# Performance work log

Measured on AMD Instinct MI355X. Metric: run time of the kernel, lower is better.

## Reference

```python
import jax, jax.numpy as jnp
import numpy as np

# Grid / problem constants
D = H = W_SP = 128      # spatial_shape of the sparse tensor (single batch)
N = 200_000             # number of active voxels
C = 64                  # nchan
K = 5                   # SubMConv3d kernel_size
PAD = 2                 # padding (stride=1 submanifold => output sites == input sites)
EPS = 1e-5              # BatchNorm eps (torch default)


def setup_inputs() -> dict:
    key = jax.random.key(0)
    k1, k2, k3 = jax.random.split(key, 3)
    # unique active voxel coordinates: permute linear grid indices, take first N
    lin = jax.random.permutation(k1, D * H * W_SP)[:N]
    z = lin // (H * W_SP)
    y = (lin // W_SP) % H
    x = lin % W_SP
    coords = jnp.stack([z, y, x], axis=1).astype(jnp.int32)   # [N,3]
    feats = jax.random.normal(k2, (N, C), jnp.float32)        # [N,C]
    std = (2.0 / (K ** 3 * C)) ** 0.5
    Wt = jax.random.normal(k3, (K ** 3, C, C), jnp.float32) * std  # [125,Cin,Cout]
    bias = jnp.full((C,), -0.01, jnp.float32)
    gamma = jnp.ones((C,), jnp.float32)   # bn weight (init 1)
    beta = jnp.zeros((C,), jnp.float32)   # bn bias (init 0)
    return {"feats": feats, "coords": coords, "Wt": Wt, "bias": bias,
            "gamma": gamma, "beta": beta}


def _subm_conv(feats, coords, Wt, bias):
    """Submanifold sparse 3D conv: out[p] = sum_k W_k @ feat[p + off_k], active only."""
    lin = (coords[:, 0] * H + coords[:, 1]) * W_SP + coords[:, 2]
    # dense hash: grid position -> active-voxel row index (or -1)
    idx_map = jnp.full((D * H * W_SP,), -1, jnp.int32).at[lin].set(
        jnp.arange(N, dtype=jnp.int32))
    r = jnp.arange(-PAD, PAD + 1)
    offs = jnp.stack(jnp.meshgrid(r, r, r, indexing="ij"), axis=-1)
    offs = offs.reshape(-1, 3).astype(jnp.int32)              # [125,3]
    bounds = jnp.array([D, H, W_SP], jnp.int32)

    def step(acc, kw):
        Wk, off = kw                                          # [C,C], [3]
        nb = coords + off                                     # [N,3]
        valid = jnp.all((nb >= 0) & (nb < bounds), axis=1)    # [N]
        nlin = (nb[:, 0] * H + nb[:, 1]) * W_SP + nb[:, 2]
        j = idx_map[jnp.where(valid, nlin, 0)]                # [N]
        ok = valid & (j >= 0)
        f = jnp.where(ok[:, None], feats[jnp.maximum(j, 0)], 0.0)  # gather [N,C]
        return acc + f @ Wk, None

    acc0 = jnp.zeros((N, C), feats.dtype)
    out, _ = jax.lax.scan(step, acc0, (Wt, offs))
    return out + bias


def reference(feats, coords, Wt, bias, gamma, beta):
    h = _subm_conv(feats, coords, Wt, bias)
    # BatchNorm1d over active voxels (training-mode batch statistics)
    mean = h.mean(axis=0)
    var = ((h - mean) ** 2).mean(axis=0)
    h = (h - mean) * jax.lax.rsqrt(var + EPS) * gamma + beta
    return jax.nn.elu(h)
```

## Files before the change

### kernel.cpp

```cpp
#include <hip/hip_runtime.h>
#include <hip/hip_bf16.h>

#define NVOX 200000
#define NK   125
#define KG   5
#define GRID_LIN (128 * 128 * 128)

#define WT_OFF    0u
#define STATS_OFF 1024000u
#define PFX_OFF   1024512u
#define OLD_OFF   1032704u
#define FB_OFF    1832704u
#define IDX_OFF   27432832u

#define F16N   (NVOX * 16)
#define WCONV_N (NK * 4096)
#define PREP_N (F16N + 16 + WCONV_N)

typedef short bf16x8 __attribute__((ext_vector_type(8)));
typedef float f32x4  __attribute__((ext_vector_type(4)));
typedef unsigned short u16x4 __attribute__((ext_vector_type(4)));
typedef unsigned int uint_as1 __attribute__((address_space(1)));
typedef unsigned int uint_as3 __attribute__((address_space(3)));

static __device__ __forceinline__ unsigned short f2bf(float f) {
    union { float f; unsigned int u; } v; v.f = f;
    unsigned int u = v.u;
    return (unsigned short)((u + 0x7FFFu + ((u >> 16) & 1u)) >> 16);
}

__global__ __launch_bounds__(256) void scatter_kernel(const int* __restrict__ coords,
                                                      int* __restrict__ idx_map) {
    int p = blockIdx.x * 256 + threadIdx.x;
    if (p < NVOX) {
        int z = coords[p * 3 + 0], y = coords[p * 3 + 1], x = coords[p * 3 + 2];
        idx_map[(z << 14) | (y << 7) | x] = p;
    }
}

__global__ __launch_bounds__(1024) void count_kernel(const int* __restrict__ idx_map,
                                                     int* __restrict__ pfx) {
    __shared__ int wsum[16];
    int i = blockIdx.x * 1024 + threadIdx.x;
    int bit = idx_map[i] >= 0 ? 1 : 0;
    unsigned long long m = __ballot(bit);
    int lane = threadIdx.x & 63, wave = threadIdx.x >> 6;
    if (lane == 0) wsum[wave] = __popcll(m);
    __syncthreads();
    if (threadIdx.x == 0) {
        int s = 0;
#pragma unroll
        for (int w = 0; w < 16; ++w) s += wsum[w];
        pfx[blockIdx.x] = s;
    }
}

__global__ __launch_bounds__(1024) void scan_kernel(int* __restrict__ pfx) {
    __shared__ int A[2048], B[2048];
    int t = threadIdx.x;
    A[t] = pfx[t]; A[t + 1024] = pfx[t + 1024];
    __syncthreads();
    int* src = A; int* dst = B;
    for (int off = 1; off < 2048; off <<= 1) {
        dst[t]        = src[t]        + (t >= off ? src[t - off] : 0);
        dst[t + 1024] = src[t + 1024] + src[t + 1024 - off];
        __syncthreads();
        int* tmp = src; src = dst; dst = tmp;
    }
    pfx[t]        = t ? src[t - 1] : 0;
    pfx[t + 1024] = src[t + 1023];
}

__global__ __launch_bounds__(1024) void relabel_kernel(const int* __restrict__ pfx,
                                                       int* __restrict__ idx_map,
                                                       int* __restrict__ oldof) {
    __shared__ int wsum[16];
    int i = blockIdx.x * 1024 + threadIdx.x;
    int old = idx_map[i];
    int bit = old >= 0 ? 1 : 0;
    unsigned long long m = __ballot(bit);
    int lane = threadIdx.x & 63, wave = threadIdx.x >> 6;
    int intra = __popcll(m & ((1ull << lane) - 1ull));
    if (lane == 0) wsum[wave] = __popcll(m);
    __syncthreads();
    int woff = 0;
    for (int w = 0; w < wave; ++w) woff += wsum[w];
    if (bit) {
        int nid = pfx[blockIdx.x] + woff + intra;
        idx_map[i] = nid;
        oldof[nid] = old;
    }
}

__global__ __launch_bounds__(256) void prep_kernel(const float* __restrict__ Wt,
                                                   const float* __restrict__ feats,
                                                   const int* __restrict__ oldof,
                                                   unsigned short* __restrict__ wt,
                                                   unsigned short* __restrict__ fb) {
    int i = blockIdx.x * 256 + threadIdx.x;
    if (i < F16N) {
        int p = i >> 4, c = i & 15;
        int old = oldof[p];
        f32x4 f = *(const f32x4*)(feats + (size_t)old * 64 + c * 4);
        u16x4 u;
        u[0] = f2bf(f[0]); u[1] = f2bf(f[1]); u[2] = f2bf(f[2]); u[3] = f2bf(f[3]);
        *(u16x4*)(fb + (size_t)i * 4) = u;
    } else if (i < F16N + 16) {
        *(u16x4*)(fb + (size_t)i * 4) = (u16x4)0;
    } else if (i < PREP_N) {
        int j = i - (F16N + 16);
        int k = j >> 12, r = j & 4095;
        int co = r >> 6, ci = r & 63;
        int dst = (co << 6) | ((((ci >> 3) ^ (co & 7)) << 3) | (ci & 7));
        wt[(k << 12) + dst] = f2bf(Wt[(k << 12) + (ci << 6) + co]);
    }
}

static __device__ __forceinline__ void stage_w(const unsigned short* wt, int k,
                                               unsigned short* dst, int tid) {
    const unsigned short* src = wt + ((size_t)k << 12) + tid * 8;
    __builtin_amdgcn_global_load_lds((const uint_as1*)(const void*)src,
                                     (uint_as3*)(void*)(dst + tid * 8), 16, 0, 0);
    __builtin_amdgcn_global_load_lds((const uint_as1*)(const void*)(src + 2048),
                                     (uint_as3*)(void*)(dst + tid * 8 + 2048), 16, 0, 0);
}

__global__ __launch_bounds__(256, 3) void conv_kernel(
    const int* __restrict__ coords, const unsigned short* __restrict__ fb,
    const unsigned short* __restrict__ wt, const int* __restrict__ idx_map,
    const int* __restrict__ oldof,
    float* __restrict__ out, float* __restrict__ stats) {
    __shared__ unsigned short lds_w[KG * 4096];
    __shared__ int lds_nbr[KG * 256];

    const int vblk = (blockIdx.x & 7) * 98 + (blockIdx.x >> 3);
    const int vbase = vblk * 256;
    if (vbase >= NVOX) return;

    const int tid  = threadIdx.x;
    const int wave = tid >> 6;
    const int lane = tid & 63;
    const int g    = lane >> 4;
    const int l15  = lane & 15;
    const int vox  = vbase + tid;
    const bool live = vox < NVOX;

    int z = 0, y = 0, x = 0;
    if (live) {
        int old = oldof[vox];
        z = coords[old * 3 + 0]; y = coords[old * 3 + 1]; x = coords[old * 3 + 2];
    }
    const int slot = (tid & ~63) | ((tid & 15) << 2) | ((tid >> 4) & 3);
    const int sw0 = ((g    ) ^ (l15 & 7)) << 4;
    const int sw1 = ((g + 4) ^ (l15 & 7)) << 4;

    f32x4 acc[4][4];
#pragma unroll
    for (int a = 0; a < 4; ++a)
#pragma unroll
        for (int b = 0; b < 4; ++b) acc[a][b] = (f32x4)0.0f;

    const char* fbp = (const char*)fb;

    for (int grp = 0; grp < NK / KG; ++grp) {
        __syncthreads();
#pragma unroll
        for (int kk = 0; kk < KG; ++kk)
            stage_w(wt, grp * KG + kk, &lds_w[kk * 4096], tid);
        const int dz = grp / 5 - 2, dy = grp % 5 - 2;
        const int nz = z + dz, ny = y + dy;
        const bool rowok = live && ((unsigned)nz < 128u) && ((unsigned)ny < 128u);
        const int base = (nz << 14) | (ny << 7);
#pragma unroll
        for (int kk = 0; kk < KG; ++kk) {
            int nx = x + kk - 2;
            int j = NVOX;
            if (rowok && ((unsigned)nx < 128u)) {
                int t = idx_map[base | nx];
                if (t >= 0) j = t;
            }
            lds_nbr[kk * 256 + slot] = j;
        }
        __syncthreads();

        int4 jt4 = *(const int4*)&lds_nbr[wave * 64 + l15 * 4];
#pragma unroll
        for (int kk = 0; kk < KG; ++kk) {
            const int jt[4] = {jt4.x, jt4.y, jt4.z, jt4.w};

            bf16x8 b0f[4], b1f[4];
#pragma unroll
            for (int t = 0; t < 4; ++t) {
                const char* rp = fbp + ((size_t)(unsigned)jt[t] << 7) + (g << 4);
                b0f[t] = *(const bf16x8*)(rp);
                b1f[t] = *(const bf16x8*)(rp + 64);
            }
            if (kk + 1 < KG)
                jt4 = *(const int4*)&lds_nbr[(kk + 1) * 256 + wave * 64 + l15 * 4];

            const char* wb = (const char*)&lds_w[kk * 4096];
            bf16x8 af0[4], af1[4];
#pragma unroll
            for (int a = 0; a < 4; ++a) {
                af0[a] = *(const bf16x8*)(wb + (((a * 16 + l15) << 7) | sw0));
                af1[a] = *(const bf16x8*)(wb + (((a * 16 + l15) << 7) | sw1));
            }

            __builtin_amdgcn_sched_barrier(0);

#pragma unroll
            for (int t = 0; t < 4; ++t) {
                if (__any(jt[t] != NVOX)) {
#pragma unroll
                    for (int a = 0; a < 4; ++a) {
                        acc[a][t] = __builtin_amdgcn_mfma_f32_16x16x32_bf16(af0[a], b0f[t], acc[a][t], 0, 0, 0);
                        acc[a][t] = __builtin_amdgcn_mfma_f32_16x16x32_bf16(af1[a], b1f[t], acc[a][t], 0, 0, 0);
                    }
                }
            }
        }
    }

#pragma unroll
    for (int b = 0; b < 4; ++b) {
        int v = vbase + wave * 64 + b * 16 + l15;
        if (v < NVOX) {
            int o = oldof[v];
#pragma unroll
            for (int a = 0; a < 4; ++a)
                *(f32x4*)(out + (size_t)o * 64 + a * 16 + g * 4) = acc[a][b];
        }
    }

    float s1[16], s2[16];
#pragma unroll
    for (int a = 0; a < 4; ++a)
#pragma unroll
        for (int r = 0; r < 4; ++r) {
            float s = 0.f, q = 0.f;
#pragma unroll
            for (int b = 0; b < 4; ++b) { float xv = acc[a][b][r]; s += xv; q += xv * xv; }
            s1[a * 4 + r] = s; s2[a * 4 + r] = q;
        }
#pragma unroll
    for (int m = 1; m < 16; m <<= 1) {
#pragma unroll
        for (int i = 0; i < 16; ++i) {
            s1[i] += __shfl_xor(s1[i], m, 64);
            s2[i] += __shfl_xor(s2[i], m, 64);
        }
    }
    if (l15 == 0) {
#pragma unroll
        for (int a = 0; a < 4; ++a)
#pragma unroll
            for (int r = 0; r < 4; ++r) {
                int co = a * 16 + g * 4 + r;
                atomicAdd(&stats[co],      s1[a * 4 + r]);
                atomicAdd(&stats[64 + co], s2[a * 4 + r]);
            }
    }
}

__global__ __launch_bounds__(256) void finalize_kernel(float* __restrict__ out,
                                                       const float* __restrict__ stats,
                                                       const float* __restrict__ gamma,
                                                       const float* __restrict__ beta) {
    int i = blockIdx.x * 256 + threadIdx.x;
    if (i >= NVOX * 16) return;
    int cg = (i & 15) * 4;
    f32x4 v = *(f32x4*)(out + (size_t)i * 4);
    f32x4 r;
#pragma unroll
    for (int c = 0; c < 4; ++c) {
        int co = cg + c;
        float mean = stats[co] * (1.0f / NVOX);
        float var  = stats[64 + co] * (1.0f / NVOX) - mean * mean;
        float sc   = rsqrtf(var + 1e-5f) * gamma[co];
        float sh   = beta[co] - mean * sc;
        float yv   = v[c] * sc + sh;
        r[c] = yv > 0.f ? yv : expm1f(yv);
    }
    *(f32x4*)(out + (size_t)i * 4) = r;
}

extern "C" void kernel_launch(void* const* d_in, const int* in_sizes, int n_in,
                              void* d_out, int out_size, void* d_ws, size_t ws_size,
                              hipStream_t stream) {
    const float* feats  = (const float*)d_in[0];
    const int*   coords = (const int*)d_in[1];
    const float* Wt     = (const float*)d_in[2];
    const float* gamma  = (const float*)d_in[4];
    const float* beta   = (const float*)d_in[5];
    float* out = (float*)d_out;
    char*  ws  = (char*)d_ws;

    unsigned short* wt  = (unsigned short*)(ws + WT_OFF);
    float* stats        = (float*)(ws + STATS_OFF);
    int*   pfx          = (int*)(ws + PFX_OFF);
    int*   oldof        = (int*)(ws + OLD_OFF);
    unsigned short* fb  = (unsigned short*)(ws + FB_OFF);
    int*   idx_map      = (int*)(ws + IDX_OFF);

    hipMemsetAsync(idx_map, 0xFF, (size_t)GRID_LIN * 4, stream);
    hipMemsetAsync(stats, 0, 128 * 4, stream);

    scatter_kernel<<<(NVOX + 255) / 256, 256, 0, stream>>>(coords, idx_map);
    count_kernel<<<GRID_LIN / 1024, 1024, 0, stream>>>(idx_map, pfx);
    scan_kernel<<<1, 1024, 0, stream>>>(pfx);
    relabel_kernel<<<GRID_LIN / 1024, 1024, 0, stream>>>(pfx, idx_map, oldof);
    prep_kernel<<<(PREP_N + 255) / 256, 256, 0, stream>>>(Wt, feats, oldof, wt, fb);
    conv_kernel<<<784, 256, 0, stream>>>(coords, fb, wt, idx_map, oldof, out, stats);
    finalize_kernel<<<12500, 256, 0, stream>>>(out, stats, gamma, beta);
}
```

Measured before the change: 700.5 us.

## Double-buffer neighbor feature gathers, rotate kernel-offset order per block, raise MFMA priority

The neighbor feature gathers for the next kernel offset are now issued before the MFMAs of the current offset, using a two-slot register buffer, so global load latency overlaps with matrix math. Each block starts its pass over the 25 offset rows at a different position (vblk mod 25), which spreads weight and idx_map accesses across blocks. MFMA sections are wrapped in s_setprio, and launch bounds drop from 3 to 2 blocks per SM to leave room for the extra live registers. The cost is higher register pressure and lower occupancy, which could hide less latency than before.

```diff
diff --git a/kernel.cpp b/kernel.cpp
--- a/kernel.cpp
+++ b/kernel.cpp
@@ -125,7 +125,7 @@
                                      (uint_as3*)(void*)(dst + tid * 8 + 2048), 16, 0, 0);
 }
 
-__global__ __launch_bounds__(256, 3) void conv_kernel(
+__global__ __launch_bounds__(256, 2) void conv_kernel(
     const int* __restrict__ coords, const unsigned short* __restrict__ fb,
     const unsigned short* __restrict__ wt, const int* __restrict__ idx_map,
     const int* __restrict__ oldof,
@@ -144,6 +144,7 @@
     const int l15  = lane & 15;
     const int vox  = vbase + tid;
     const bool live = vox < NVOX;
+    const int rot  = vblk % 25;
 
     int z = 0, y = 0, x = 0;
     if (live) {
@@ -163,11 +164,12 @@
     const char* fbp = (const char*)fb;
 
     for (int grp = 0; grp < NK / KG; ++grp) {
+        int ge = grp + rot; if (ge >= 25) ge -= 25;
         __syncthreads();
 #pragma unroll
         for (int kk = 0; kk < KG; ++kk)
-            stage_w(wt, grp * KG + kk, &lds_w[kk * 4096], tid);
-        const int dz = grp / 5 - 2, dy = grp % 5 - 2;
+            stage_w(wt, ge * KG + kk, &lds_w[kk * 4096], tid);
+        const int dz = ge / 5 - 2, dy = ge % 5 - 2;
         const int nz = z + dz, ny = y + dy;
         const bool rowok = live && ((unsigned)nz < 128u) && ((unsigned)ny < 128u);
         const int base = (nz << 14) | (ny << 7);
@@ -183,21 +185,31 @@
         }
         __syncthreads();
 
-        int4 jt4 = *(const int4*)&lds_nbr[wave * 64 + l15 * 4];
+        int    jj[2][4];
+        bf16x8 bb[2][8];
+        {
+            int4 q = *(const int4*)&lds_nbr[wave * 64 + l15 * 4];
+            jj[0][0] = q.x; jj[0][1] = q.y; jj[0][2] = q.z; jj[0][3] = q.w;
+#pragma unroll
+            for (int t = 0; t < 4; ++t) {
+                const char* rp = fbp + ((size_t)(unsigned)jj[0][t] << 7) + (g << 4);
+                bb[0][t * 2]     = *(const bf16x8*)(rp);
+                bb[0][t * 2 + 1] = *(const bf16x8*)(rp + 64);
+            }
+        }
 #pragma unroll
         for (int kk = 0; kk < KG; ++kk) {
-            const int jt[4] = {jt4.x, jt4.y, jt4.z, jt4.w};
-
-            bf16x8 b0f[4], b1f[4];
-#pragma unroll
-            for (int t = 0; t < 4; ++t) {
-                const char* rp = fbp + ((size_t)(unsigned)jt[t] << 7) + (g << 4);
-                b0f[t] = *(const bf16x8*)(rp);
-                b1f[t] = *(const bf16x8*)(rp + 64);
-            }
-            if (kk + 1 < KG)
-                jt4 = *(const int4*)&lds_nbr[(kk + 1) * 256 + wave * 64 + l15 * 4];
-
+            const int cur = kk & 1, nxt = cur ^ 1;
+            if (kk + 1 < KG) {
+                int4 q = *(const int4*)&lds_nbr[(kk + 1) * 256 + wave * 64 + l15 * 4];
+                jj[nxt][0] = q.x; jj[nxt][1] = q.y; jj[nxt][2] = q.z; jj[nxt][3] = q.w;
+#pragma unroll
+                for (int t = 0; t < 4; ++t) {
+                    const char* rp = fbp + ((size_t)(unsigned)jj[nxt][t] << 7) + (g << 4);
+                    bb[nxt][t * 2]     = *(const bf16x8*)(rp);
+                    bb[nxt][t * 2 + 1] = *(const bf16x8*)(rp + 64);
+                }
+            }
             const char* wb = (const char*)&lds_w[kk * 4096];
             bf16x8 af0[4], af1[4];
 #pragma unroll
@@ -205,19 +217,19 @@
                 af0[a] = *(const bf16x8*)(wb + (((a * 16 + l15) << 7) | sw0));
                 af1[a] = *(const bf16x8*)(wb + (((a * 16 + l15) << 7) | sw1));
             }
-
             __builtin_amdgcn_sched_barrier(0);
-
+            __builtin_amdgcn_s_setprio(1);
 #pragma unroll
             for (int t = 0; t < 4; ++t) {
-                if (__any(jt[t] != NVOX)) {
+                if (__any(jj[cur][t] != NVOX)) {
 #pragma unroll
                     for (int a = 0; a < 4; ++a) {
-                        acc[a][t] = __builtin_amdgcn_mfma_f32_16x16x32_bf16(af0[a], b0f[t], acc[a][t], 0, 0, 0);
-                        acc[a][t] = __builtin_amdgcn_mfma_f32_16x16x32_bf16(af1[a], b1f[t], acc[a][t], 0, 0, 0);
+                        acc[a][t] = __builtin_amdgcn_mfma_f32_16x16x32_bf16(af0[a], bb[cur][t * 2],     acc[a][t], 0, 0, 0);
+                        acc[a][t] = __builtin_amdgcn_mfma_f32_16x16x32_bf16(af1[a], bb[cur][t * 2 + 1], acc[a][t], 0, 0, 0);
                     }
                 }
             }
+            __builtin_amdgcn_s_setprio(0);
         }
     }
 
```

Result: faster. 641.1 us (-8.5%).

## Compact active neighbor pairs per offset and accumulate conv outputs in LDS

Applied to the files above, without the earlier changes.

Replaces the dense per-offset MFMA over all 256 voxels with a ballot-compacted list of (neighbor, voxel) pairs for each kernel offset. Only tiles of real active pairs are multiplied, and the results are scattered into an LDS fp32 accumulator with atomics. Weight staging through LDS is removed: weights are read directly from global/L2 in plain layout, and the block's offset order is rotated to spread accesses. This targets the wasted gathers and MFMAs on empty neighbors. In exchange it adds two block barriers per offset, LDS atomics, poor wave balance on small pair counts, and a larger LDS footprint that lowers occupancy.

```diff
diff --git a/kernel.cpp b/kernel.cpp
--- a/kernel.cpp
+++ b/kernel.cpp
@@ -3,8 +3,8 @@
 
 #define NVOX 200000
 #define NK   125
-#define KG   5
 #define GRID_LIN (128 * 128 * 128)
+#define ASTRIDE 68
 
 #define WT_OFF    0u
 #define STATS_OFF 1024000u
@@ -20,8 +20,6 @@
 typedef short bf16x8 __attribute__((ext_vector_type(8)));
 typedef float f32x4  __attribute__((ext_vector_type(4)));
 typedef unsigned short u16x4 __attribute__((ext_vector_type(4)));
-typedef unsigned int uint_as1 __attribute__((address_space(1)));
-typedef unsigned int uint_as3 __attribute__((address_space(3)));
 
 static __device__ __forceinline__ unsigned short f2bf(float f) {
     union { float f; unsigned int u; } v; v.f = f;
@@ -111,27 +109,18 @@
         int j = i - (F16N + 16);
         int k = j >> 12, r = j & 4095;
         int co = r >> 6, ci = r & 63;
-        int dst = (co << 6) | ((((ci >> 3) ^ (co & 7)) << 3) | (ci & 7));
-        wt[(k << 12) + dst] = f2bf(Wt[(k << 12) + (ci << 6) + co]);
-    }
-}
-
-static __device__ __forceinline__ void stage_w(const unsigned short* wt, int k,
-                                               unsigned short* dst, int tid) {
-    const unsigned short* src = wt + ((size_t)k << 12) + tid * 8;
-    __builtin_amdgcn_global_load_lds((const uint_as1*)(const void*)src,
-                                     (uint_as3*)(void*)(dst + tid * 8), 16, 0, 0);
-    __builtin_amdgcn_global_load_lds((const uint_as1*)(const void*)(src + 2048),
-                                     (uint_as3*)(void*)(dst + tid * 8 + 2048), 16, 0, 0);
-}
-
-__global__ __launch_bounds__(256, 3) void conv_kernel(
+        wt[(k << 12) + (co << 6) + ci] = f2bf(Wt[(k << 12) + (ci << 6) + co]);
+    }
+}
+
+__global__ __launch_bounds__(256, 2) void conv_kernel(
     const int* __restrict__ coords, const unsigned short* __restrict__ fb,
     const unsigned short* __restrict__ wt, const int* __restrict__ idx_map,
     const int* __restrict__ oldof,
     float* __restrict__ out, float* __restrict__ stats) {
-    __shared__ unsigned short lds_w[KG * 4096];
-    __shared__ int lds_nbr[KG * 256];
+    __shared__ float accum[256 * ASTRIDE];
+    __shared__ unsigned int plist[256];
+    __shared__ int pcnt2[2];
 
     const int vblk = (blockIdx.x & 7) * 98 + (blockIdx.x >> 3);
     const int vbase = vblk * 256;
@@ -144,121 +133,95 @@
     const int l15  = lane & 15;
     const int vox  = vbase + tid;
     const bool live = vox < NVOX;
+    const int rot  = vblk % 25;
 
     int z = 0, y = 0, x = 0;
     if (live) {
         int old = oldof[vox];
         z = coords[old * 3 + 0]; y = coords[old * 3 + 1]; x = coords[old * 3 + 2];
     }
-    const int slot = (tid & ~63) | ((tid & 15) << 2) | ((tid >> 4) & 3);
-    const int sw0 = ((g    ) ^ (l15 & 7)) << 4;
-    const int sw1 = ((g + 4) ^ (l15 & 7)) << 4;
-
-    f32x4 acc[4][4];
-#pragma unroll
-    for (int a = 0; a < 4; ++a)
-#pragma unroll
-        for (int b = 0; b < 4; ++b) acc[a][b] = (f32x4)0.0f;
+
+    {
+        f32x4* az = (f32x4*)accum;
+#pragma unroll
+        for (int i = 0; i < 17; ++i) az[i * 256 + tid] = (f32x4)0.0f;
+        if (tid < 2) pcnt2[tid] = 0;
+    }
+    __syncthreads();
 
     const char* fbp = (const char*)fb;
-
-    for (int grp = 0; grp < NK / KG; ++grp) {
-        __syncthreads();
-#pragma unroll
-        for (int kk = 0; kk < KG; ++kk)
-            stage_w(wt, grp * KG + kk, &lds_w[kk * 4096], tid);
-        const int dz = grp / 5 - 2, dy = grp % 5 - 2;
+    const char* wtp = (const char*)wt;
+
+    for (int grp = 0; grp < 25; ++grp) {
+        int ge = grp + rot; if (ge >= 25) ge -= 25;
+        const int dz = ge / 5 - 2, dy = ge % 5 - 2;
         const int nz = z + dz, ny = y + dy;
         const bool rowok = live && ((unsigned)nz < 128u) && ((unsigned)ny < 128u);
         const int base = (nz << 14) | (ny << 7);
-#pragma unroll
-        for (int kk = 0; kk < KG; ++kk) {
+#pragma unroll 1
+        for (int kk = 0; kk < 5; ++kk) {
+            const int k  = ge * 5 + kk;
+            const int it = grp * 5 + kk;
+            int j = -1;
             int nx = x + kk - 2;
-            int j = NVOX;
-            if (rowok && ((unsigned)nx < 128u)) {
-                int t = idx_map[base | nx];
-                if (t >= 0) j = t;
+            if (rowok && ((unsigned)nx < 128u)) j = idx_map[base | nx];
+            unsigned long long m = __ballot(j >= 0);
+            int intra = __popcll(m & ((1ull << lane) - 1ull));
+            int wcnt  = __popcll(m);
+            int wbase = 0;
+            if (lane == 0 && wcnt) wbase = atomicAdd(&pcnt2[it & 1], wcnt);
+            wbase = __shfl(wbase, 0, 64);
+            if (j >= 0) plist[wbase + intra] = ((unsigned)j << 9) | (unsigned)tid;
+            __syncthreads();
+
+            const int cnt = pcnt2[it & 1];
+            const int nt  = (cnt + 15) >> 4;
+            for (int t = wave; t < nt; t += 4) {
+                int pi = t * 16 + l15;
+                unsigned e = (pi < cnt) ? plist[pi] : ((unsigned)NVOX << 9);
+                int pj   = (int)(e >> 9);
+                int slot = (int)(e & 511u);
+                const char* rp = fbp + ((size_t)(unsigned)pj << 7) + (g << 4);
+                bf16x8 b0 = *(const bf16x8*)(rp);
+                bf16x8 b1 = *(const bf16x8*)(rp + 64);
+                const char* wb = wtp + ((size_t)k << 13) + (l15 << 7) + (g << 4);
+                f32x4 c[4];
+#pragma unroll
+                for (int a = 0; a < 4; ++a) {
+                    bf16x8 a0 = *(const bf16x8*)(wb + a * 2048);
+                    bf16x8 a1 = *(const bf16x8*)(wb + a * 2048 + 64);
+                    c[a] = (f32x4)0.0f;
+                    c[a] = __builtin_amdgcn_mfma_f32_16x16x32_bf16(a0, b0, c[a], 0, 0, 0);
+                    c[a] = __builtin_amdgcn_mfma_f32_16x16x32_bf16(a1, b1, c[a], 0, 0, 0);
+                }
+                float* arow = &accum[slot * ASTRIDE];
+#pragma unroll
+                for (int a = 0; a < 4; ++a)
+#pragma unroll
+                    for (int r = 0; r < 4; ++r)
+                        atomicAdd(&arow[a * 16 + g * 4 + r], c[a][r]);
             }
-            lds_nbr[kk * 256 + slot] = j;
+            __syncthreads();
+            if (tid == 0) pcnt2[it & 1] = 0;
         }
-        __syncthreads();
-
-        int4 jt4 = *(const int4*)&lds_nbr[wave * 64 + l15 * 4];
-#pragma unroll
-        for (int kk = 0; kk < KG; ++kk) {
-            const int jt[4] = {jt4.x, jt4.y, jt4.z, jt4.w};
-
-            bf16x8 b0f[4], b1f[4];
-#pragma unroll
-            for (int t = 0; t < 4; ++t) {
-                const char* rp = fbp + ((size_t)(unsigned)jt[t] << 7) + (g << 4);
-                b0f[t] = *(const bf16x8*)(rp);
-                b1f[t] = *(const bf16x8*)(rp + 64);
-            }
-            if (kk + 1 < KG)
-                jt4 = *(const int4*)&lds_nbr[(kk + 1) * 256 + wave * 64 + l15 * 4];
-
-            const char* wb = (const char*)&lds_w[kk * 4096];
-            bf16x8 af0[4], af1[4];
-#pragma unroll
-            for (int a = 0; a < 4; ++a) {
-                af0[a] = *(const bf16x8*)(wb + (((a * 16 + l15) << 7) | sw0));
-                af1[a] = *(const bf16x8*)(wb + (((a * 16 + l15) << 7) | sw1));
-            }
-
-            __builtin_amdgcn_sched_barrier(0);
-
-#pragma unroll
-            for (int t = 0; t < 4; ++t) {
-                if (__any(jt[t] != NVOX)) {
-#pragma unroll
-                    for (int a = 0; a < 4; ++a) {
-                        acc[a][t] = __builtin_amdgcn_mfma_f32_16x16x32_bf16(af0[a], b0f[t], acc[a][t], 0, 0, 0);
-                        acc[a][t] = __builtin_amdgcn_mfma_f32_16x16x32_bf16(af1[a], b1f[t], acc[a][t], 0, 0, 0);
-                    }
-                }
-            }
+    }
+
+    {
+        float s = 0.f, q = 0.f;
+        for (int i = 0; i < 64; ++i) {
+            float v = accum[(wave * 64 + i) * ASTRIDE + lane];
+            s += v; q += v * v;
         }
-    }
-
-#pragma unroll
-    for (int b = 0; b < 4; ++b) {
-        int v = vbase + wave * 64 + b * 16 + l15;
-        if (v < NVOX) {
-            int o = oldof[v];
-#pragma unroll
-            for (int a = 0; a < 4; ++a)
-                *(f32x4*)(out + (size_t)o * 64 + a * 16 + g * 4) = acc[a][b];
-        }
-    }
-
-    float s1[16], s2[16];
-#pragma unroll
-    for (int a = 0; a < 4; ++a)
-#pragma unroll
-        for (int r = 0; r < 4; ++r) {
-            float s = 0.f, q = 0.f;
-#pragma unroll
-            for (int b = 0; b < 4; ++b) { float xv = acc[a][b][r]; s += xv; q += xv * xv; }
-            s1[a * 4 + r] = s; s2[a * 4 + r] = q;
-        }
-#pragma unroll
-    for (int m = 1; m < 16; m <<= 1) {
-#pragma unroll
-        for (int i = 0; i < 16; ++i) {
-            s1[i] += __shfl_xor(s1[i], m, 64);
-            s2[i] += __shfl_xor(s2[i], m, 64);
-        }
-    }
-    if (l15 == 0) {
-#pragma unroll
-        for (int a = 0; a < 4; ++a)
-#pragma unroll
-            for (int r = 0; r < 4; ++r) {
-                int co = a * 16 + g * 4 + r;
-                atomicAdd(&stats[co],      s1[a * 4 + r]);
-                atomicAdd(&stats[64 + co], s2[a * 4 + r]);
-            }
+        atomicAdd(&stats[lane], s);
+        atomicAdd(&stats[64 + lane], q);
+    }
+
+    if (live) {
+        int o = oldof[vox];
+        const float* arow = &accum[tid * ASTRIDE];
+#pragma unroll
+        for (int a2 = 0; a2 < 16; ++a2)
+            *(f32x4*)(out + (size_t)o * 64 + a2 * 4) = *(const f32x4*)(arow + a2 * 4);
     }
 }
 
```

After: 1.880 ms. +168.4%, slower.

## Replace LDS-staged weights and neighbor tables with register-pipelined gathers and direct weight loads

Applied to the files above, without the earlier changes.

Removes the shared-memory staging of weights and neighbor indices along with both block barriers per offset group. Neighbor probes now run two offsets ahead and feature gathers one offset ahead in registers, double-buffered across a hand-pipelined loop. Weights are read straight from global memory (via cache) in an unswizzled layout, and neighbor indices are broadcast with wave shuffles. This trades LDS traffic and barrier stalls for more register pressure and per-wave global or L2 weight reads.

```diff
diff --git a/kernel.cpp b/kernel.cpp
--- a/kernel.cpp
+++ b/kernel.cpp
@@ -3,7 +3,6 @@
 
 #define NVOX 200000
 #define NK   125
-#define KG   5
 #define GRID_LIN (128 * 128 * 128)
 
 #define WT_OFF    0u
@@ -20,8 +19,6 @@
 typedef short bf16x8 __attribute__((ext_vector_type(8)));
 typedef float f32x4  __attribute__((ext_vector_type(4)));
 typedef unsigned short u16x4 __attribute__((ext_vector_type(4)));
-typedef unsigned int uint_as1 __attribute__((address_space(1)));
-typedef unsigned int uint_as3 __attribute__((address_space(3)));
 
 static __device__ __forceinline__ unsigned short f2bf(float f) {
     union { float f; unsigned int u; } v; v.f = f;
@@ -111,27 +108,60 @@
         int j = i - (F16N + 16);
         int k = j >> 12, r = j & 4095;
         int co = r >> 6, ci = r & 63;
-        int dst = (co << 6) | ((((ci >> 3) ^ (co & 7)) << 3) | (ci & 7));
-        wt[(k << 12) + dst] = f2bf(Wt[(k << 12) + (ci << 6) + co]);
-    }
-}
-
-static __device__ __forceinline__ void stage_w(const unsigned short* wt, int k,
-                                               unsigned short* dst, int tid) {
-    const unsigned short* src = wt + ((size_t)k << 12) + tid * 8;
-    __builtin_amdgcn_global_load_lds((const uint_as1*)(const void*)src,
-                                     (uint_as3*)(void*)(dst + tid * 8), 16, 0, 0);
-    __builtin_amdgcn_global_load_lds((const uint_as1*)(const void*)(src + 2048),
-                                     (uint_as3*)(void*)(dst + tid * 8 + 2048), 16, 0, 0);
-}
+        wt[(k << 12) + (co << 6) + ci] = f2bf(Wt[(k << 12) + (ci << 6) + co]);
+    }
+}
+
+#define PROBE(kk, dst) do {                                                  \
+    int k_ = (kk);                                                           \
+    dst = -1;                                                                \
+    if (k_ < NK) {                                                           \
+        int dz_ = (k_ * 41) >> 10; int r_ = k_ - dz_ * 25;                   \
+        int dy_ = (r_ * 205) >> 10; int dx_ = r_ - dy_ * 5;                  \
+        int nz_ = z + dz_ - 2, ny_ = y + dy_ - 2, nx_ = x + dx_ - 2;         \
+        if (live && ((unsigned)nz_ < 128u) && ((unsigned)ny_ < 128u)         \
+                 && ((unsigned)nx_ < 128u))                                  \
+            dst = idx_map[(nz_ << 14) | (ny_ << 7) | nx_];                   \
+    }                                                                        \
+} while (0)
+
+#define GATHER(jsrc, jt, bb) do {                                            \
+    _Pragma("unroll")                                                        \
+    for (int t_ = 0; t_ < 4; ++t_) {                                         \
+        int jv_ = __shfl(jsrc, t_ * 16 + l15, 64);                           \
+        jt[t_] = (jv_ < 0) ? NVOX : jv_;                                     \
+        const char* rp_ = fbp + ((size_t)(unsigned)jt[t_] << 7) + (g << 4);  \
+        bb[t_ * 2]     = *(const bf16x8*)(rp_);                              \
+        bb[t_ * 2 + 1] = *(const bf16x8*)(rp_ + 64);                         \
+    }                                                                        \
+} while (0)
+
+#define COMPUTE(k_, jt, bb) do {                                             \
+    const char* wb_ = wtp + ((size_t)(k_) << 13) + (l15 << 7) + (g << 4);    \
+    bool kt_[4];                                                             \
+    _Pragma("unroll")                                                        \
+    for (int t_ = 0; t_ < 4; ++t_) kt_[t_] = __any(jt[t_] != NVOX);          \
+    _Pragma("unroll")                                                        \
+    for (int a_ = 0; a_ < 4; ++a_) {                                         \
+        bf16x8 a0_ = *(const bf16x8*)(wb_ + a_ * 2048);                      \
+        bf16x8 a1_ = *(const bf16x8*)(wb_ + a_ * 2048 + 64);                 \
+        _Pragma("unroll")                                                    \
+        for (int t_ = 0; t_ < 4; ++t_) {                                     \
+            if (kt_[t_]) {                                                   \
+                acc[a_][t_] = __builtin_amdgcn_mfma_f32_16x16x32_bf16(       \
+                    a0_, bb[t_ * 2], acc[a_][t_], 0, 0, 0);                  \
+                acc[a_][t_] = __builtin_amdgcn_mfma_f32_16x16x32_bf16(       \
+                    a1_, bb[t_ * 2 + 1], acc[a_][t_], 0, 0, 0);              \
+            }                                                                \
+        }                                                                    \
+    }                                                                        \
+} while (0)
 
 __global__ __launch_bounds__(256, 3) void conv_kernel(
     const int* __restrict__ coords, const unsigned short* __restrict__ fb,
     const unsigned short* __restrict__ wt, const int* __restrict__ idx_map,
     const int* __restrict__ oldof,
     float* __restrict__ out, float* __restrict__ stats) {
-    __shared__ unsigned short lds_w[KG * 4096];
-    __shared__ int lds_nbr[KG * 256];
 
     const int vblk = (blockIdx.x & 7) * 98 + (blockIdx.x >> 3);
     const int vbase = vblk * 256;
@@ -150,9 +180,6 @@
         int old = oldof[vox];
         z = coords[old * 3 + 0]; y = coords[old * 3 + 1]; x = coords[old * 3 + 2];
     }
-    const int slot = (tid & ~63) | ((tid & 15) << 2) | ((tid >> 4) & 3);
-    const int sw0 = ((g    ) ^ (l15 & 7)) << 4;
-    const int sw1 = ((g + 4) ^ (l15 & 7)) << 4;
 
     f32x4 acc[4][4];
 #pragma unroll
@@ -161,65 +188,30 @@
         for (int b = 0; b < 4; ++b) acc[a][b] = (f32x4)0.0f;
 
     const char* fbp = (const char*)fb;
-
-    for (int grp = 0; grp < NK / KG; ++grp) {
-        __syncthreads();
-#pragma unroll
-        for (int kk = 0; kk < KG; ++kk)
-            stage_w(wt, grp * KG + kk, &lds_w[kk * 4096], tid);
-        const int dz = grp / 5 - 2, dy = grp % 5 - 2;
-        const int nz = z + dz, ny = y + dy;
-        const bool rowok = live && ((unsigned)nz < 128u) && ((unsigned)ny < 128u);
-        const int base = (nz << 14) | (ny << 7);
-#pragma unroll
-        for (int kk = 0; kk < KG; ++kk) {
-            int nx = x + kk - 2;
-            int j = NVOX;
-            if (rowok && ((unsigned)nx < 128u)) {
-                int t = idx_map[base | nx];
-                if (t >= 0) j = t;
-            }
-            lds_nbr[kk * 256 + slot] = j;
-        }
-        __syncthreads();
-
-        int4 jt4 = *(const int4*)&lds_nbr[wave * 64 + l15 * 4];
-#pragma unroll
-        for (int kk = 0; kk < KG; ++kk) {
-            const int jt[4] = {jt4.x, jt4.y, jt4.z, jt4.w};
-
-            bf16x8 b0f[4], b1f[4];
-#pragma unroll
-            for (int t = 0; t < 4; ++t) {
-                const char* rp = fbp + ((size_t)(unsigned)jt[t] << 7) + (g << 4);
-                b0f[t] = *(const bf16x8*)(rp);
-                b1f[t] = *(const bf16x8*)(rp + 64);
-            }
-            if (kk + 1 < KG)
-                jt4 = *(const int4*)&lds_nbr[(kk + 1) * 256 + wave * 64 + l15 * 4];
-
-            const char* wb = (const char*)&lds_w[kk * 4096];
-            bf16x8 af0[4], af1[4];
-#pragma unroll
-            for (int a = 0; a < 4; ++a) {
-                af0[a] = *(const bf16x8*)(wb + (((a * 16 + l15) << 7) | sw0));
-                af1[a] = *(const bf16x8*)(wb + (((a * 16 + l15) << 7) | sw1));
-            }
-
-            __builtin_amdgcn_sched_barrier(0);
-
-#pragma unroll
-            for (int t = 0; t < 4; ++t) {
-                if (__any(jt[t] != NVOX)) {
-#pragma unroll
-                    for (int a = 0; a < 4; ++a) {
-                        acc[a][t] = __builtin_amdgcn_mfma_f32_16x16x32_bf16(af0[a], b0f[t], acc[a][t], 0, 0, 0);
-                        acc[a][t] = __builtin_amdgcn_mfma_f32_16x16x32_bf16(af1[a], b1f[t], acc[a][t], 0, 0, 0);
-                    }
-                }
-            }
-        }
-    }
+    const char* wtp = (const char*)wt;
+
+    int jtA[4], jtB[4];
+    bf16x8 bbA[8], bbB[8];
+    int j0, jB, jC, jD, jE;
+
+    PROBE(0, j0); PROBE(1, jB); PROBE(2, jC);
+    GATHER(j0, jtA, bbA);
+
+#pragma unroll 1
+    for (int k = 0; k < 124; k += 2) {
+        PROBE(k + 3, jD);
+        GATHER(jB, jtB, bbB);
+        __builtin_amdgcn_sched_barrier(0);
+        COMPUTE(k, jtA, bbA);
+
+        PROBE(k + 4, jE);
+        GATHER(jC, jtA, bbA);
+        __builtin_amdgcn_sched_barrier(0);
+        COMPUTE(k + 1, jtB, bbB);
+
+        jB = jD; jC = jE;
+    }
+    COMPUTE(124, jtA, bbA);
 
 #pragma unroll
     for (int b = 0; b < 4; ++b) {
```

After: 1.125 ms. +60.6%, slower.
